# Kernel tuning notes

Hardware: AMD Instinct MI355X
Metric: run time of the kernel (lower is better)

Reference implementation:

```python
import jax, jax.numpy as jnp
from jax import lax
import numpy as np

STATE_DIM = 64
CHANNELS = 128
SEQ_LEN = 4096
BATCH = 16
DT_MIN, DT_MAX = 1e-3, 1e-1


def hippo(n):
    # HiPPO-LegS construction, matching the torch staticmethod
    ar = jnp.arange(n, dtype=jnp.float32)
    P = jnp.sqrt(1.0 + 2.0 * ar)
    A = P[:, None] * P[None, :]
    A = jnp.tril(A) - jnp.diag(ar)
    B = jnp.sqrt(2.0 * ar + 1.0)
    return -A, B[:, None]


def setup_inputs() -> dict:
    key = jax.random.key(0)
    k_u, k_c = jax.random.split(key)
    A, B = hippo(STATE_DIM)
    # xavier_normal_ for C: std = sqrt(2/(fan_in+fan_out))
    std = float(np.sqrt(2.0 / (CHANNELS + STATE_DIM)))
    C = jax.random.normal(k_c, (CHANNELS, STATE_DIM), dtype=jnp.float32) * std
    D = jnp.ones((CHANNELS, 1), dtype=jnp.float32)
    # deterministic dt at log-midpoint of [dt_min, dt_max]
    dt = jnp.exp(jnp.array([(np.log(DT_MIN) + np.log(DT_MAX)) / 2.0], dtype=jnp.float32))
    u = jax.random.normal(k_u, (BATCH, SEQ_LEN), dtype=jnp.float32)
    return {"u": u, "A": A, "B": B, "C": C, "D": D, "dt": dt}


def reference(u, A, B, C, D, dt):
    # Training-path forward of LinearStateSpaceLayer (conv-kernel construction + conv1d)
    b, L = u.shape
    n = A.shape[0]
    dt_s = dt[0]
    I = jnp.eye(n, dtype=A.dtype)
    BL = jnp.linalg.inv(I - 0.5 * dt_s * A)            # bilinear discretization
    A_bar = BL @ (I + 0.5 * dt_s * A)                  # (n, n)
    B_bar = (BL * dt_s) @ B                            # (n, 1)

    # kernel k[j] = C @ A_bar^j @ B_bar for j = 0..L-1, via a scan of matvecs
    def step(v, _):
        return A_bar @ v, v
    _, vs = lax.scan(step, B_bar[:, 0], None, length=L)  # (L, n), vs[j] = A_bar^j B_bar
    k_causal = vs @ C.T                                  # (L, channels)
    # torch ordering: k_conv[c, 0, i] = C A_bar^{L-1-i} B_bar = k_causal[L-1-i, c]
    k_conv = k_causal[::-1].T[:, None, :]                # (channels, 1, L)

    # torch F.conv1d is cross-correlation; lax conv_general_dilated matches
    y = lax.conv_general_dilated(
        u[:, None, :], k_conv,
        window_strides=(1,), padding=[(L - 1, L - 1)],
        dimension_numbers=("NCH", "OIH", "NCH"),
    )[:, :, :L]                                          # (b, channels, L)

    # skip term: (u.unsqueeze(-1) @ D.T).transpose(-1,-2) == u[b,t] * D[c,0]
    y = y + u[:, None, :] * D[None, :, :]                # (b, channels, L)
    return y
```

## Files before the change

kernel.cpp:

```cpp
#include <hip/hip_runtime.h>

#define NS   64
#define CH   128
#define LSEQ 4096
#define NB   16
#define SCH  64
#define MCH  64
#define ST   68
#define CP   128

#define WS_ABAR 0
#define WS_A16  4096
#define WS_VS   8192
#define WS_BBAR 12288

#define X0_IDX(b, m) (((size_t)(b) * CH) * LSEQ + (size_t)(m) * SCH)

#define P_VSS  0
#define P_XCW  1024
#define P_XBS  1280
#define P_PLE  1536
#define P_PART 1792
#define P_A16  2048

#define FMA44(av, bv)                                                          \
    a0.x += av.x * bv.x; a0.y += av.x * bv.y; a0.z += av.x * bv.z; a0.w += av.x * bv.w; \
    a1.x += av.y * bv.x; a1.y += av.y * bv.y; a1.z += av.y * bv.z; a1.w += av.y * bv.w; \
    a2.x += av.z * bv.x; a2.y += av.z * bv.y; a2.z += av.z * bv.z; a2.w += av.z * bv.w; \
    a3.x += av.w * bv.x; a3.y += av.w * bv.y; a3.z += av.w * bv.z; a3.w += av.w * bv.w;

__global__ __launch_bounds__(512) void k_sb(const float* __restrict__ u,
                                            const float* __restrict__ A,
                                            const float* __restrict__ Bv,
                                            const float* __restrict__ dtp,
                                            float* __restrict__ ws,
                                            float* __restrict__ out) {
    __shared__ __align__(16) float Mrow[NS * ST];
    __shared__ __align__(16) float Mcol[(NS + 1) * ST];
    __shared__ __align__(16) float Nrow[NS * ST];
    __shared__ __align__(16) float Ncol[NS * ST];
    __shared__ __align__(16) float VT[NS * ST];
    __shared__ __align__(16) float vsS[NS * NS];
    __shared__ __align__(16) float xleS[MCH * NS];
    __shared__ __align__(16) float part[2][4 * NS];
    __shared__ __align__(16) float bcol[NS];
    __shared__ float rdiag[NS], xcS[NS];
    const int tid = threadIdx.x;
    const int b = blockIdx.x;
    const float dt = dtp[0];
    const float hdt = 0.5f * dt;

    for (int o = tid; o < NS * ST; o += 512) { Mrow[o] = 0.f; Nrow[o] = 0.f; Ncol[o] = 0.f; VT[o] = 0.f; }
    for (int o = tid; o < (NS + 1) * ST; o += 512) Mcol[o] = 0.f;
    __syncthreads();

    for (int o = tid; o < NS * NS; o += 512) {
        int i = o >> 6, k = o & 63;
        float a = A[o];
        float d = (i == k) ? 1.0f : 0.0f;
        Nrow[i * ST + k] = d - hdt * a;
        Ncol[k * ST + i] = d + hdt * a;
    }
    if (tid < NS) {
        bcol[tid]  = dt * Bv[tid];
        rdiag[tid] = 1.0f / (1.0f - hdt * A[tid * NS + tid]);
    }
    __syncthreads();

    if (tid <= NS) {
        float xr[NS];
        const float* t2b = (tid < NS) ? &Ncol[tid * ST] : bcol;
#pragma unroll
        for (int I = 0; I < 16; ++I) {
            const int i0 = 4 * I;
            float4 t2 = *(const float4*)&t2b[i0];
            float a0 = t2.x, a1 = t2.y, a2 = t2.z, a3 = t2.w;
#pragma unroll
            for (int k = 0; k < i0; k += 4) {
                float4 n0 = *(const float4*)&Nrow[(i0 + 0) * ST + k];
                float4 n1 = *(const float4*)&Nrow[(i0 + 1) * ST + k];
                float4 n2 = *(const float4*)&Nrow[(i0 + 2) * ST + k];
                float4 n3 = *(const float4*)&Nrow[(i0 + 3) * ST + k];
                a0 -= n0.x * xr[k] + n0.y * xr[k + 1] + n0.z * xr[k + 2] + n0.w * xr[k + 3];
                a1 -= n1.x * xr[k] + n1.y * xr[k + 1] + n1.z * xr[k + 2] + n1.w * xr[k + 3];
                a2 -= n2.x * xr[k] + n2.y * xr[k + 1] + n2.z * xr[k + 2] + n2.w * xr[k + 3];
                a3 -= n3.x * xr[k] + n3.y * xr[k + 1] + n3.z * xr[k + 2] + n3.w * xr[k + 3];
            }
            float4 rd  = *(const float4*)&rdiag[i0];
            float4 nb1 = *(const float4*)&Nrow[(i0 + 1) * ST + i0];
            float4 nb2 = *(const float4*)&Nrow[(i0 + 2) * ST + i0];
            float4 nb3 = *(const float4*)&Nrow[(i0 + 3) * ST + i0];
            float x0 = a0 * rd.x;
            float x1 = (a1 - nb1.x * x0) * rd.y;
            float x2 = (a2 - nb2.x * x0 - nb2.y * x1) * rd.z;
            float x3 = (a3 - nb3.x * x0 - nb3.y * x1 - nb3.z * x2) * rd.w;
            xr[i0 + 0] = x0; xr[i0 + 1] = x1; xr[i0 + 2] = x2; xr[i0 + 3] = x3;
        }
        float* xrow = &Mcol[tid * ST];
#pragma unroll
        for (int k = 0; k < NS; k += 4) {
            float4 v = {xr[k], xr[k + 1], xr[k + 2], xr[k + 3]};
            *(float4*)&xrow[k] = v;
        }
    }
    __syncthreads();

    if (tid < 256) {
        const int i0 = 4 * (tid >> 4), j0 = 4 * (tid & 15);
        float4 r0 = *(const float4*)&Mcol[(j0 + 0) * ST + i0];
        float4 r1 = *(const float4*)&Mcol[(j0 + 1) * ST + i0];
        float4 r2 = *(const float4*)&Mcol[(j0 + 2) * ST + i0];
        float4 r3 = *(const float4*)&Mcol[(j0 + 3) * ST + i0];
        float4 w0 = {r0.x, r1.x, r2.x, r3.x};
        float4 w1 = {r0.y, r1.y, r2.y, r3.y};
        float4 w2 = {r0.z, r1.z, r2.z, r3.z};
        float4 w3 = {r0.w, r1.w, r2.w, r3.w};
        *(float4*)&Mrow[(i0 + 0) * ST + j0] = w0;
        *(float4*)&Mrow[(i0 + 1) * ST + j0] = w1;
        *(float4*)&Mrow[(i0 + 2) * ST + j0] = w2;
        *(float4*)&Mrow[(i0 + 3) * ST + j0] = w3;
        if (b == 0) {
            *(float4*)&ws[WS_ABAR + (i0 + 0) * NS + j0] = w0;
            *(float4*)&ws[WS_ABAR + (i0 + 1) * NS + j0] = w1;
            *(float4*)&ws[WS_ABAR + (i0 + 2) * NS + j0] = w2;
            *(float4*)&ws[WS_ABAR + (i0 + 3) * NS + j0] = w3;
        }
    }
    if (b == 0 && tid < 16)
        *(float4*)&ws[WS_BBAR + 4 * tid] = *(const float4*)&Mcol[NS * ST + 4 * tid];
    if (tid < NS) VT[tid * ST + 0] = Mcol[NS * ST + tid];
    __syncthreads();

    float *cm = Mrow, *cmt = Mcol, *nm = Nrow, *nmt = Ncol;
    const int l = tid & 63;
    const int si0 = 16 * ((tid >> 6) & 3) + 4 * (l >> 4);
    const int sj0 = 4 * (l & 15);
    for (int s = 1; s <= 6; ++s) {
        if (tid < 256) {
            float4 a0 = {0,0,0,0}, a1 = {0,0,0,0}, a2 = {0,0,0,0}, a3 = {0,0,0,0};
#pragma unroll 4
            for (int k = 0; k < NS; k += 4) {
                float4 av0 = *(const float4*)&cmt[(k + 0) * ST + si0];
                float4 bv0 = *(const float4*)&cm [(k + 0) * ST + sj0];
                float4 av1 = *(const float4*)&cmt[(k + 1) * ST + si0];
                float4 bv1 = *(const float4*)&cm [(k + 1) * ST + sj0];
                float4 av2 = *(const float4*)&cmt[(k + 2) * ST + si0];
                float4 bv2 = *(const float4*)&cm [(k + 2) * ST + sj0];
                float4 av3 = *(const float4*)&cmt[(k + 3) * ST + si0];
                float4 bv3 = *(const float4*)&cm [(k + 3) * ST + sj0];
                FMA44(av0, bv0)
                FMA44(av1, bv1)
                FMA44(av2, bv2)
                FMA44(av3, bv3)
            }
            *(float4*)&nm[(si0 + 0) * ST + sj0] = a0;
            *(float4*)&nm[(si0 + 1) * ST + sj0] = a1;
            *(float4*)&nm[(si0 + 2) * ST + sj0] = a2;
            *(float4*)&nm[(si0 + 3) * ST + sj0] = a3;
            float4 t0 = {a0.x, a1.x, a2.x, a3.x};
            float4 t1 = {a0.y, a1.y, a2.y, a3.y};
            float4 t2 = {a0.z, a1.z, a2.z, a3.z};
            float4 t3 = {a0.w, a1.w, a2.w, a3.w};
            *(float4*)&nmt[(sj0 + 0) * ST + si0] = t0;
            *(float4*)&nmt[(sj0 + 1) * ST + si0] = t1;
            *(float4*)&nmt[(sj0 + 2) * ST + si0] = t2;
            *(float4*)&nmt[(sj0 + 3) * ST + si0] = t3;
        } else {
            const int e = tid - 256;
            if (s == 1) {
                if (e < NS) {
                    float sum = 0.f;
#pragma unroll 8
                    for (int k = 0; k < NS; ++k) sum += cmt[k * ST + e] * VT[k * ST + 0];
                    VT[e * ST + 1] = sum;
                }
            } else if (s == 2) {
                if (e < 2 * NS) {
                    const int i = e & 63, j = e >> 6;
                    float sum = 0.f;
#pragma unroll 8
                    for (int k = 0; k < NS; ++k) sum += cmt[k * ST + i] * VT[k * ST + j];
                    VT[i * ST + 2 + j] = sum;
                }
            } else {
                const int mexp = 1 << (s - 1);
                if (e < 4 * mexp) {
                    const int vi = 4 * (e & 15), vj = 4 * (e >> 4);
                    float4 a0 = {0,0,0,0}, a1 = {0,0,0,0}, a2 = {0,0,0,0}, a3 = {0,0,0,0};
#pragma unroll 4
                    for (int k = 0; k < NS; k += 2) {
                        float4 av  = *(const float4*)&cmt[k * ST + vi];
                        float4 bv  = *(const float4*)&VT [k * ST + vj];
                        float4 av2 = *(const float4*)&cmt[(k + 1) * ST + vi];
                        float4 bv2 = *(const float4*)&VT [(k + 1) * ST + vj];
                        FMA44(av, bv)
                        FMA44(av2, bv2)
                    }
                    *(float4*)&VT[(vi + 0) * ST + vj + mexp] = a0;
                    *(float4*)&VT[(vi + 1) * ST + vj + mexp] = a1;
                    *(float4*)&VT[(vi + 2) * ST + vj + mexp] = a2;
                    *(float4*)&VT[(vi + 3) * ST + vj + mexp] = a3;
                }
            }
        }
        __syncthreads();
        { float* t = cm; cm = nm; nm = t; t = cmt; cmt = nmt; nmt = t; }
        if (s == 4 && b == 0) {
            for (int o = tid; o < (NS * NS) / 4; o += 512) {
                int r = o >> 4, c4 = (o & 15) * 4;
                *(float4*)&ws[WS_A16 + r * NS + c4] = *(const float4*)&cm[r * ST + c4];
            }
        }
    }

    if (tid < 256) {
        const int i0 = 4 * (tid >> 4), j0 = 4 * (tid & 15);
        float4 v0 = *(const float4*)&VT[(i0 + 0) * ST + j0];
        float4 v1 = *(const float4*)&VT[(i0 + 1) * ST + j0];
        float4 v2 = *(const float4*)&VT[(i0 + 2) * ST + j0];
        float4 v3 = *(const float4*)&VT[(i0 + 3) * ST + j0];
        float4 w0 = {v0.x, v1.x, v2.x, v3.x};
        float4 w1 = {v0.y, v1.y, v2.y, v3.y};
        float4 w2 = {v0.z, v1.z, v2.z, v3.z};
        float4 w3 = {v0.w, v1.w, v2.w, v3.w};
        *(float4*)&vsS[(j0 + 0) * NS + i0] = w0;
        *(float4*)&vsS[(j0 + 1) * NS + i0] = w1;
        *(float4*)&vsS[(j0 + 2) * NS + i0] = w2;
        *(float4*)&vsS[(j0 + 3) * NS + i0] = w3;
        if (b == 0) {
            *(float4*)&ws[WS_VS + (j0 + 0) * NS + i0] = w0;
            *(float4*)&ws[WS_VS + (j0 + 1) * NS + i0] = w1;
            *(float4*)&ws[WS_VS + (j0 + 2) * NS + i0] = w2;
            *(float4*)&ws[WS_VS + (j0 + 3) * NS + i0] = w3;
        }
    }
    {
        const int jj = tid & 63;
#pragma unroll
        for (int rep = 0; rep < 2; ++rep) {
            const int m0 = 4 * (tid >> 6) + 32 * rep;
            float4 v;
            v.x = u[b * LSEQ + (m0 + 0) * SCH + 63 - jj];
            v.y = u[b * LSEQ + (m0 + 1) * SCH + 63 - jj];
            v.z = u[b * LSEQ + (m0 + 2) * SCH + 63 - jj];
            v.w = u[b * LSEQ + (m0 + 3) * SCH + 63 - jj];
            *(float4*)&Nrow[jj * ST + m0] = v;
        }
    }
    const int i = tid & 63, q = (tid >> 6) & 3;
    float4 a64[4];
    if (tid < 256) {
#pragma unroll
        for (int kq = 0; kq < 4; ++kq)
            a64[kq] = *(const float4*)&Mrow[i * ST + 16 * q + 4 * kq];
    }
    if (tid < NS) xcS[tid] = 0.f;
    __syncthreads();

    if (tid < 256) {
        const int ig = tid & 15, mg = tid >> 4;
        float4 a0 = {0,0,0,0}, a1 = {0,0,0,0}, a2 = {0,0,0,0}, a3 = {0,0,0,0};
#pragma unroll 4
        for (int j = 0; j < NS; j += 2) {
            float4 am  = *(const float4*)&Nrow[j * ST + 4 * mg];
            float4 bi  = *(const float4*)&vsS[j * NS + 4 * ig];
            float4 am2 = *(const float4*)&Nrow[(j + 1) * ST + 4 * mg];
            float4 bi2 = *(const float4*)&vsS[(j + 1) * NS + 4 * ig];
            FMA44(am, bi)
            FMA44(am2, bi2)
        }
        *(float4*)&xleS[(4 * mg + 0) * NS + 4 * ig] = a0;
        *(float4*)&xleS[(4 * mg + 1) * NS + 4 * ig] = a1;
        *(float4*)&xleS[(4 * mg + 2) * NS + 4 * ig] = a2;
        *(float4*)&xleS[(4 * mg + 3) * NS + 4 * ig] = a3;
    }
    __syncthreads();

    for (int m = 0; m < MCH; ++m) {
        if (tid < 256) {
            if (q == 0 && tid < 64) out[X0_IDX(b, m) + i] = xcS[i];
            float4 t0 = *(const float4*)(xcS + 16 * q + 0);
            float4 t1 = *(const float4*)(xcS + 16 * q + 4);
            float4 t2 = *(const float4*)(xcS + 16 * q + 8);
            float4 t3 = *(const float4*)(xcS + 16 * q + 12);
            float s = a64[0].x * t0.x + a64[0].y * t0.y + a64[0].z * t0.z + a64[0].w * t0.w
                    + a64[1].x * t1.x + a64[1].y * t1.y + a64[1].z * t1.z + a64[1].w * t1.w
                    + a64[2].x * t2.x + a64[2].y * t2.y + a64[2].z * t2.z + a64[2].w * t2.w
                    + a64[3].x * t3.x + a64[3].y * t3.y + a64[3].z * t3.z + a64[3].w * t3.w;
            part[m & 1][q * 64 + i] = s;
        }
        __syncthreads();
        if (tid < 256) {
            float xn = part[m & 1][i] + part[m & 1][64 + i] + part[m & 1][128 + i]
                     + part[m & 1][192 + i] + xleS[m * 64 + i];
            xcS[i] = xn;
        }
    }
}

__global__ __launch_bounds__(256) void k_main2(const float* __restrict__ u,
                                               const float* __restrict__ Cm,
                                               const float* __restrict__ Dv,
                                               const float* __restrict__ ws,
                                               float* __restrict__ out) {
    __shared__ __align__(16) float Xl[NS * ST];
    __shared__ __align__(16) float pool[NS * CP];
    __shared__ float uS[SCH], DS[CH], bbS[NS];
    const int m = blockIdx.x, b = blockIdx.y;
    const int tid = threadIdx.x;
    const int l = tid & 63, w = tid >> 6;

    for (int o = tid; o < (NS * NS) / 4; o += 256) {
        int r = o >> 4, c4 = (o & 15) * 4;
        *(float4*)&Xl[r * ST + c4]          = *(const float4*)&ws[WS_ABAR + r * NS + c4];
        *(float4*)&pool[P_A16 + r * NS + c4] = *(const float4*)&ws[WS_A16 + r * NS + c4];
    }
    for (int o = tid; o < 16 * NS; o += 256) pool[P_VSS + o] = ws[WS_VS + o];
    if (tid < NS) {
        uS[tid]  = u[b * LSEQ + m * SCH + tid];
        bbS[tid] = ws[WS_BBAR + tid];
        pool[P_XBS + tid] = out[X0_IDX(b, m) + tid];
    }
    if (tid < CH) DS[tid] = Dv[tid];
    __syncthreads();

    const int r0 = l & 15, q = l >> 4;
    float4 ar[4][4];
#pragma unroll
    for (int b4 = 0; b4 < 4; ++b4)
#pragma unroll
        for (int kq = 0; kq < 4; ++kq)
            ar[b4][kq] = *(const float4*)&Xl[(r0 + 16 * b4) * ST + 16 * q + 4 * kq];
    float bbr[4];
#pragma unroll
    for (int b4 = 0; b4 < 4; ++b4) bbr[b4] = bbS[r0 + 16 * b4];
    float4 a16r[4];
#pragma unroll
    for (int kq = 0; kq < 4; ++kq)
        a16r[kq] = *(const float4*)&pool[P_A16 + l * NS + 16 * w + 4 * kq];

    {
        float s = 0.f;
#pragma unroll
        for (int j = 0; j < 16; ++j) s += pool[P_VSS + j * NS + l] * uS[16 * w + 15 - j];
        pool[P_PLE + w * NS + l] = s;
    }
    __syncthreads();

    for (int p = 1; p < 4; ++p) {
        float4 x0q = *(const float4*)&pool[P_XBS + (p - 1) * NS + 16 * w + 0];
        float4 x1q = *(const float4*)&pool[P_XBS + (p - 1) * NS + 16 * w + 4];
        float4 x2q = *(const float4*)&pool[P_XBS + (p - 1) * NS + 16 * w + 8];
        float4 x3q = *(const float4*)&pool[P_XBS + (p - 1) * NS + 16 * w + 12];
        float s = a16r[0].x * x0q.x + a16r[0].y * x0q.y + a16r[0].z * x0q.z + a16r[0].w * x0q.w
                + a16r[1].x * x1q.x + a16r[1].y * x1q.y + a16r[1].z * x1q.z + a16r[1].w * x1q.w
                + a16r[2].x * x2q.x + a16r[2].y * x2q.y + a16r[2].z * x2q.z + a16r[2].w * x2q.w
                + a16r[3].x * x3q.x + a16r[3].y * x3q.y + a16r[3].z * x3q.z + a16r[3].w * x3q.w;
        pool[P_PART + w * NS + l] = s;
        __syncthreads();
        if (w == 0) {
            float xn = pool[P_PART + l] + pool[P_PART + NS + l] + pool[P_PART + 2 * NS + l]
                     + pool[P_PART + 3 * NS + l] + pool[P_PLE + (p - 1) * NS + l];
            pool[P_XBS + p * NS + l] = xn;
        }
        __syncthreads();
    }

    pool[P_XCW + w * NS + l] = pool[P_XBS + w * NS + l];
    for (int s = 0; s < 16; ++s) {
        __threadfence_block();
        const int t = 16 * w + s;
        float4 x0q = *(const float4*)&pool[P_XCW + w * NS + 16 * q + 0];
        float4 x1q = *(const float4*)&pool[P_XCW + w * NS + 16 * q + 4];
        float4 x2q = *(const float4*)&pool[P_XCW + w * NS + 16 * q + 8];
        float4 x3q = *(const float4*)&pool[P_XCW + w * NS + 16 * q + 12];
        float p0, p1, p2, p3;
        p0 = ar[0][0].x * x0q.x + ar[0][0].y * x0q.y + ar[0][0].z * x0q.z + ar[0][0].w * x0q.w
           + ar[0][1].x * x1q.x + ar[0][1].y * x1q.y + ar[0][1].z * x1q.z + ar[0][1].w * x1q.w
           + ar[0][2].x * x2q.x + ar[0][2].y * x2q.y + ar[0][2].z * x2q.z + ar[0][2].w * x2q.w
           + ar[0][3].x * x3q.x + ar[0][3].y * x3q.y + ar[0][3].z * x3q.z + ar[0][3].w * x3q.w;
        p1 = ar[1][0].x * x0q.x + ar[1][0].y * x0q.y + ar[1][0].z * x0q.z + ar[1][0].w * x0q.w
           + ar[1][1].x * x1q.x + ar[1][1].y * x1q.y + ar[1][1].z * x1q.z + ar[1][1].w * x1q.w
           + ar[1][2].x * x2q.x + ar[1][2].y * x2q.y + ar[1][2].z * x2q.z + ar[1][2].w * x2q.w
           + ar[1][3].x * x3q.x + ar[1][3].y * x3q.y + ar[1][3].z * x3q.z + ar[1][3].w * x3q.w;
        p2 = ar[2][0].x * x0q.x + ar[2][0].y * x0q.y + ar[2][0].z * x0q.z + ar[2][0].w * x0q.w
           + ar[2][1].x * x1q.x + ar[2][1].y * x1q.y + ar[2][1].z * x1q.z + ar[2][1].w * x1q.w
           + ar[2][2].x * x2q.x + ar[2][2].y * x2q.y + ar[2][2].z * x2q.z + ar[2][2].w * x2q.w
           + ar[2][3].x * x3q.x + ar[2][3].y * x3q.y + ar[2][3].z * x3q.z + ar[2][3].w * x3q.w;
        p3 = ar[3][0].x * x0q.x + ar[3][0].y * x0q.y + ar[3][0].z * x0q.z + ar[3][0].w * x0q.w
           + ar[3][1].x * x1q.x + ar[3][1].y * x1q.y + ar[3][1].z * x1q.z + ar[3][1].w * x1q.w
           + ar[3][2].x * x2q.x + ar[3][2].y * x2q.y + ar[3][2].z * x2q.z + ar[3][2].w * x2q.w
           + ar[3][3].x * x3q.x + ar[3][3].y * x3q.y + ar[3][3].z * x3q.z + ar[3][3].w * x3q.w;
        p0 += __shfl_xor(p0, 16, 64); p1 += __shfl_xor(p1, 16, 64);
        p2 += __shfl_xor(p2, 16, 64); p3 += __shfl_xor(p3, 16, 64);
        p0 += __shfl_xor(p0, 32, 64); p1 += __shfl_xor(p1, 32, 64);
        p2 += __shfl_xor(p2, 32, 64); p3 += __shfl_xor(p3, 32, 64);
        const float ut = uS[t];
        p0 += bbr[0] * ut; p1 += bbr[1] * ut; p2 += bbr[2] * ut; p3 += bbr[3] * ut;
        const float xv = (q == 0) ? p0 : (q == 1) ? p1 : (q == 2) ? p2 : p3;
        const int row = r0 + 16 * q;
        pool[P_XCW + w * NS + row] = xv;
        Xl[row * ST + t] = xv;
    }
    __syncthreads();

#pragma unroll
    for (int rep = 0; rep < 8; ++rep) {
        const int ii = tid & 63;
        const int cg = (tid >> 6) + 4 * rep;
        float4 v;
        v.x = Cm[(4 * cg + 0) * NS + ii];
        v.y = Cm[(4 * cg + 1) * NS + ii];
        v.z = Cm[(4 * cg + 2) * NS + ii];
        v.w = Cm[(4 * cg + 3) * NS + ii];
        *(float4*)&pool[ii * CP + 4 * cg] = v;
    }
    __syncthreads();

    {
        const int tg = tid & 7, cq = tid >> 3;
        float acc[4][8];
#pragma unroll
        for (int r = 0; r < 4; ++r)
#pragma unroll
            for (int c = 0; c < 8; ++c) acc[r][c] = 0.f;
#pragma unroll 4
        for (int ii = 0; ii < NS; ++ii) {
            float4 cv = *(const float4*)&pool[ii * CP + 4 * cq];
            float4 xa = *(const float4*)&Xl[ii * ST + 8 * tg + 0];
            float4 xb = *(const float4*)&Xl[ii * ST + 8 * tg + 4];
            float cr[4] = {cv.x, cv.y, cv.z, cv.w};
            float xv[8] = {xa.x, xa.y, xa.z, xa.w, xb.x, xb.y, xb.z, xb.w};
#pragma unroll
            for (int r = 0; r < 4; ++r)
#pragma unroll
                for (int c = 0; c < 8; ++c) acc[r][c] += cr[r] * xv[c];
        }
        const size_t obase = ((size_t)b * CH) * LSEQ + (size_t)m * SCH + 8 * tg;
#pragma unroll
        for (int r = 0; r < 4; ++r) {
            const int c = 4 * cq + r;
            const float dv = DS[c];
            float4 o1, o2;
            o1.x = acc[r][0] + dv * uS[8 * tg + 0];
            o1.y = acc[r][1] + dv * uS[8 * tg + 1];
            o1.z = acc[r][2] + dv * uS[8 * tg + 2];
            o1.w = acc[r][3] + dv * uS[8 * tg + 3];
            o2.x = acc[r][4] + dv * uS[8 * tg + 4];
            o2.y = acc[r][5] + dv * uS[8 * tg + 5];
            o2.z = acc[r][6] + dv * uS[8 * tg + 6];
            o2.w = acc[r][7] + dv * uS[8 * tg + 7];
            float* op = out + obase + (size_t)c * LSEQ;
            *(float4*)(op)     = o1;
            *(float4*)(op + 4) = o2;
        }
    }
}

extern "C" void kernel_launch(void* const* d_in, const int* in_sizes, int n_in,
                              void* d_out, int out_size, void* d_ws, size_t ws_size,
                              hipStream_t stream) {
    const float* u   = (const float*)d_in[0];
    const float* A   = (const float*)d_in[1];
    const float* Bv  = (const float*)d_in[2];
    const float* Cm  = (const float*)d_in[3];
    const float* Dv  = (const float*)d_in[4];
    const float* dtp = (const float*)d_in[5];
    float* ws  = (float*)d_ws;
    float* out = (float*)d_out;

    k_sb<<<NB, 512, 0, stream>>>(u, A, Bv, dtp, ws, out);
    k_main2<<<dim3(MCH, NB), 256, 0, stream>>>(u, Cm, Dv, ws, out);
}
```

Before: 161.0 us.

## Replace serial chunk-state recurrence with log-depth parallel prefix scan

```diff
diff --git a/kernel.cpp b/kernel.cpp
--- a/kernel.cpp
+++ b/kernel.cpp
@@ -28,6 +28,82 @@
     a1.x += av.y * bv.x; a1.y += av.y * bv.y; a1.z += av.y * bv.z; a1.w += av.y * bv.w; \
     a2.x += av.z * bv.x; a2.y += av.z * bv.y; a2.z += av.z * bv.z; a2.w += av.z * bv.w; \
     a3.x += av.w * bv.x; a3.y += av.w * bv.y; a3.z += av.w * bv.z; a3.w += av.w * bv.w;
+
+__device__ __forceinline__ void mm_square(const float* __restrict__ cm,
+                                          const float* __restrict__ cmt,
+                                          float* __restrict__ nm,
+                                          float* __restrict__ nmt, int tid) {
+    const int l = tid & 63;
+    const int si0 = 16 * ((tid >> 6) & 3) + 4 * (l >> 4);
+    const int sj0 = 4 * (l & 15);
+    float4 a0 = {0,0,0,0}, a1 = {0,0,0,0}, a2 = {0,0,0,0}, a3 = {0,0,0,0};
+#pragma unroll 4
+    for (int k = 0; k < NS; k += 4) {
+        float4 av0 = *(const float4*)&cmt[(k + 0) * ST + si0];
+        float4 bv0 = *(const float4*)&cm [(k + 0) * ST + sj0];
+        float4 av1 = *(const float4*)&cmt[(k + 1) * ST + si0];
+        float4 bv1 = *(const float4*)&cm [(k + 1) * ST + sj0];
+        float4 av2 = *(const float4*)&cmt[(k + 2) * ST + si0];
+        float4 bv2 = *(const float4*)&cm [(k + 2) * ST + sj0];
+        float4 av3 = *(const float4*)&cmt[(k + 3) * ST + si0];
+        float4 bv3 = *(const float4*)&cm [(k + 3) * ST + sj0];
+        FMA44(av0, bv0)
+        FMA44(av1, bv1)
+        FMA44(av2, bv2)
+        FMA44(av3, bv3)
+    }
+    *(float4*)&nm[(si0 + 0) * ST + sj0] = a0;
+    *(float4*)&nm[(si0 + 1) * ST + sj0] = a1;
+    *(float4*)&nm[(si0 + 2) * ST + sj0] = a2;
+    *(float4*)&nm[(si0 + 3) * ST + sj0] = a3;
+    float4 t0 = {a0.x, a1.x, a2.x, a3.x};
+    float4 t1 = {a0.y, a1.y, a2.y, a3.y};
+    float4 t2 = {a0.z, a1.z, a2.z, a3.z};
+    float4 t3 = {a0.w, a1.w, a2.w, a3.w};
+    *(float4*)&nmt[(sj0 + 0) * ST + si0] = t0;
+    *(float4*)&nmt[(sj0 + 1) * ST + si0] = t1;
+    *(float4*)&nmt[(sj0 + 2) * ST + si0] = t2;
+    *(float4*)&nmt[(sj0 + 3) * ST + si0] = t3;
+}
+
+template<int D>
+__device__ __forceinline__ void scan_level(const float* __restrict__ PT,
+                                           const float* __restrict__ Tin,
+                                           float* __restrict__ Tout, int e) {
+    const int i0 = 4 * (e >> 4);
+    const int m0 = 4 * (e & 15);
+    float4 a0 = {0,0,0,0}, a1 = {0,0,0,0}, a2 = {0,0,0,0}, a3 = {0,0,0,0};
+    if (D < 4 || m0 >= D) {
+#pragma unroll 4
+        for (int k = 0; k < NS; ++k) {
+            float4 av = *(const float4*)&PT[k * ST + i0];
+            float4 bv;
+            if constexpr (D >= 4) {
+                bv = *(const float4*)&Tin[k * ST + m0 - D];
+            } else {
+                float4 bhi = *(const float4*)&Tin[k * ST + m0];
+                float4 blo;
+                if (m0 >= 4) blo = *(const float4*)&Tin[k * ST + m0 - 4];
+                else { blo.x = 0.f; blo.y = 0.f; blo.z = 0.f; blo.w = 0.f; }
+                if constexpr (D == 1) { bv.x = blo.w; bv.y = bhi.x; bv.z = bhi.y; bv.w = bhi.z; }
+                else                  { bv.x = blo.z; bv.y = blo.w; bv.z = bhi.x; bv.w = bhi.y; }
+            }
+            FMA44(av, bv)
+        }
+    }
+    float4 t0 = *(const float4*)&Tin[(i0 + 0) * ST + m0];
+    float4 t1 = *(const float4*)&Tin[(i0 + 1) * ST + m0];
+    float4 t2 = *(const float4*)&Tin[(i0 + 2) * ST + m0];
+    float4 t3 = *(const float4*)&Tin[(i0 + 3) * ST + m0];
+    a0.x += t0.x; a0.y += t0.y; a0.z += t0.z; a0.w += t0.w;
+    a1.x += t1.x; a1.y += t1.y; a1.z += t1.z; a1.w += t1.w;
+    a2.x += t2.x; a2.y += t2.y; a2.z += t2.z; a2.w += t2.w;
+    a3.x += t3.x; a3.y += t3.y; a3.z += t3.z; a3.w += t3.w;
+    *(float4*)&Tout[(i0 + 0) * ST + m0] = a0;
+    *(float4*)&Tout[(i0 + 1) * ST + m0] = a1;
+    *(float4*)&Tout[(i0 + 2) * ST + m0] = a2;
+    *(float4*)&Tout[(i0 + 3) * ST + m0] = a3;
+}
 
 __global__ __launch_bounds__(512) void k_sb(const float* __restrict__ u,
                                             const float* __restrict__ A,
@@ -39,12 +115,13 @@
     __shared__ __align__(16) float Mcol[(NS + 1) * ST];
     __shared__ __align__(16) float Nrow[NS * ST];
     __shared__ __align__(16) float Ncol[NS * ST];
+    __shared__ __align__(16) float Wrow[NS * ST];
+    __shared__ __align__(16) float Wcol[NS * ST];
     __shared__ __align__(16) float VT[NS * ST];
-    __shared__ __align__(16) float vsS[NS * NS];
-    __shared__ __align__(16) float xleS[MCH * NS];
-    __shared__ __align__(16) float part[2][4 * NS];
+    __shared__ __align__(16) float T1[NS * ST];
     __shared__ __align__(16) float bcol[NS];
-    __shared__ float rdiag[NS], xcS[NS];
+    __shared__ float rdiag[NS];
+    float* const vsS = Wrow;
     const int tid = threadIdx.x;
     const int b = blockIdx.x;
     const float dt = dtp[0];
@@ -132,39 +209,9 @@
     __syncthreads();
 
     float *cm = Mrow, *cmt = Mcol, *nm = Nrow, *nmt = Ncol;
-    const int l = tid & 63;
-    const int si0 = 16 * ((tid >> 6) & 3) + 4 * (l >> 4);
-    const int sj0 = 4 * (l & 15);
     for (int s = 1; s <= 6; ++s) {
         if (tid < 256) {
-            float4 a0 = {0,0,0,0}, a1 = {0,0,0,0}, a2 = {0,0,0,0}, a3 = {0,0,0,0};
-#pragma unroll 4
-            for (int k = 0; k < NS; k += 4) {
-                float4 av0 = *(const float4*)&cmt[(k + 0) * ST + si0];
-                float4 bv0 = *(const float4*)&cm [(k + 0) * ST + sj0];
-                float4 av1 = *(const float4*)&cmt[(k + 1) * ST + si0];
-                float4 bv1 = *(const float4*)&cm [(k + 1) * ST + sj0];
-                float4 av2 = *(const float4*)&cmt[(k + 2) * ST + si0];
-                float4 bv2 = *(const float4*)&cm [(k + 2) * ST + sj0];
-                float4 av3 = *(const float4*)&cmt[(k + 3) * ST + si0];
-                float4 bv3 = *(const float4*)&cm [(k + 3) * ST + sj0];
-                FMA44(av0, bv0)
-                FMA44(av1, bv1)
-                FMA44(av2, bv2)
-                FMA44(av3, bv3)
-            }
-            *(float4*)&nm[(si0 + 0) * ST + sj0] = a0;
-            *(float4*)&nm[(si0 + 1) * ST + sj0] = a1;
-            *(float4*)&nm[(si0 + 2) * ST + sj0] = a2;
-            *(float4*)&nm[(si0 + 3) * ST + sj0] = a3;
-            float4 t0 = {a0.x, a1.x, a2.x, a3.x};
-            float4 t1 = {a0.y, a1.y, a2.y, a3.y};
-            float4 t2 = {a0.z, a1.z, a2.z, a3.z};
-            float4 t3 = {a0.w, a1.w, a2.w, a3.w};
-            *(float4*)&nmt[(sj0 + 0) * ST + si0] = t0;
-            *(float4*)&nmt[(sj0 + 1) * ST + si0] = t1;
-            *(float4*)&nmt[(sj0 + 2) * ST + si0] = t2;
-            *(float4*)&nmt[(sj0 + 3) * ST + si0] = t3;
+            mm_square(cm, cmt, nm, nmt, tid);
         } else {
             const int e = tid - 256;
             if (s == 1) {
@@ -244,57 +291,78 @@
             v.y = u[b * LSEQ + (m0 + 1) * SCH + 63 - jj];
             v.z = u[b * LSEQ + (m0 + 2) * SCH + 63 - jj];
             v.w = u[b * LSEQ + (m0 + 3) * SCH + 63 - jj];
-            *(float4*)&Nrow[jj * ST + m0] = v;
-        }
-    }
-    const int i = tid & 63, q = (tid >> 6) & 3;
-    float4 a64[4];
+            *(float4*)&T1[jj * ST + m0] = v;
+        }
+    }
+    __syncthreads();
+
     if (tid < 256) {
-#pragma unroll
-        for (int kq = 0; kq < 4; ++kq)
-            a64[kq] = *(const float4*)&Mrow[i * ST + 16 * q + 4 * kq];
-    }
-    if (tid < NS) xcS[tid] = 0.f;
-    __syncthreads();
-
-    if (tid < 256) {
-        const int ig = tid & 15, mg = tid >> 4;
+        mm_square(Mrow, Mcol, Nrow, Ncol, tid);
+    } else {
+        const int e = tid - 256;
+        const int ig = e & 15, mg = e >> 4;
         float4 a0 = {0,0,0,0}, a1 = {0,0,0,0}, a2 = {0,0,0,0}, a3 = {0,0,0,0};
 #pragma unroll 4
         for (int j = 0; j < NS; j += 2) {
-            float4 am  = *(const float4*)&Nrow[j * ST + 4 * mg];
+            float4 am  = *(const float4*)&T1[j * ST + 4 * mg];
             float4 bi  = *(const float4*)&vsS[j * NS + 4 * ig];
-            float4 am2 = *(const float4*)&Nrow[(j + 1) * ST + 4 * mg];
+            float4 am2 = *(const float4*)&T1[(j + 1) * ST + 4 * mg];
             float4 bi2 = *(const float4*)&vsS[(j + 1) * NS + 4 * ig];
             FMA44(am, bi)
             FMA44(am2, bi2)
         }
-        *(float4*)&xleS[(4 * mg + 0) * NS + 4 * ig] = a0;
-        *(float4*)&xleS[(4 * mg + 1) * NS + 4 * ig] = a1;
-        *(float4*)&xleS[(4 * mg + 2) * NS + 4 * ig] = a2;
-        *(float4*)&xleS[(4 * mg + 3) * NS + 4 * ig] = a3;
-    }
-    __syncthreads();
-
-    for (int m = 0; m < MCH; ++m) {
-        if (tid < 256) {
-            if (q == 0 && tid < 64) out[X0_IDX(b, m) + i] = xcS[i];
-            float4 t0 = *(const float4*)(xcS + 16 * q + 0);
-            float4 t1 = *(const float4*)(xcS + 16 * q + 4);
-            float4 t2 = *(const float4*)(xcS + 16 * q + 8);
-            float4 t3 = *(const float4*)(xcS + 16 * q + 12);
-            float s = a64[0].x * t0.x + a64[0].y * t0.y + a64[0].z * t0.z + a64[0].w * t0.w
-                    + a64[1].x * t1.x + a64[1].y * t1.y + a64[1].z * t1.z + a64[1].w * t1.w
-                    + a64[2].x * t2.x + a64[2].y * t2.y + a64[2].z * t2.z + a64[2].w * t2.w
-                    + a64[3].x * t3.x + a64[3].y * t3.y + a64[3].z * t3.z + a64[3].w * t3.w;
-            part[m & 1][q * 64 + i] = s;
-        }
-        __syncthreads();
-        if (tid < 256) {
-            float xn = part[m & 1][i] + part[m & 1][64 + i] + part[m & 1][128 + i]
-                     + part[m & 1][192 + i] + xleS[m * 64 + i];
-            xcS[i] = xn;
-        }
+        float4 w0 = {a0.x, a1.x, a2.x, a3.x};
+        float4 w1 = {a0.y, a1.y, a2.y, a3.y};
+        float4 w2 = {a0.z, a1.z, a2.z, a3.z};
+        float4 w3 = {a0.w, a1.w, a2.w, a3.w};
+        *(float4*)&VT[(4 * ig + 0) * ST + 4 * mg] = w0;
+        *(float4*)&VT[(4 * ig + 1) * ST + 4 * mg] = w1;
+        *(float4*)&VT[(4 * ig + 2) * ST + 4 * mg] = w2;
+        *(float4*)&VT[(4 * ig + 3) * ST + 4 * mg] = w3;
+    }
+    __syncthreads();
+
+    if (tid < 256) mm_square(Nrow, Ncol, Wrow, Wcol, tid);
+    else           scan_level<1>(Mcol, VT, T1, tid - 256);
+    __syncthreads();
+
+    if (tid < 256) mm_square(Wrow, Wcol, Mrow, Mcol, tid);
+    else           scan_level<2>(Ncol, T1, VT, tid - 256);
+    __syncthreads();
+
+    if (tid < 256) mm_square(Mrow, Mcol, Nrow, Ncol, tid);
+    else           scan_level<4>(Wcol, VT, T1, tid - 256);
+    __syncthreads();
+
+    if (tid < 256) mm_square(Nrow, Ncol, Wrow, Wcol, tid);
+    else           scan_level<8>(Mcol, T1, VT, tid - 256);
+    __syncthreads();
+
+    if (tid >= 256) scan_level<16>(Ncol, VT, T1, tid - 256);
+    __syncthreads();
+
+    if (tid >= 256) scan_level<32>(Wcol, T1, VT, tid - 256);
+    __syncthreads();
+
+    {
+        const int m = tid >> 3;
+        const int i0 = (tid & 7) * 8;
+        float4 o1, o2;
+        if (m == 0) {
+            o1.x = o1.y = o1.z = o1.w = 0.f;
+            o2.x = o2.y = o2.z = o2.w = 0.f;
+        } else {
+            o1.x = VT[(i0 + 0) * ST + m - 1];
+            o1.y = VT[(i0 + 1) * ST + m - 1];
+            o1.z = VT[(i0 + 2) * ST + m - 1];
+            o1.w = VT[(i0 + 3) * ST + m - 1];
+            o2.x = VT[(i0 + 4) * ST + m - 1];
+            o2.y = VT[(i0 + 5) * ST + m - 1];
+            o2.z = VT[(i0 + 6) * ST + m - 1];
+            o2.w = VT[(i0 + 7) * ST + m - 1];
+        }
+        *(float4*)&out[X0_IDX(b, m) + i0]     = o1;
+        *(float4*)&out[X0_IDX(b, m) + i0 + 4] = o2;
     }
 }
 
```

New measurement: 171.7 us. 1.07x slower.

## Run chunk-state recurrence in a single wavefront with shuffles instead of block syncs

Applied to the files above, without the earlier changes.

```diff
diff --git a/kernel.cpp b/kernel.cpp
--- a/kernel.cpp
+++ b/kernel.cpp
@@ -40,19 +40,15 @@
     __shared__ __align__(16) float Nrow[NS * ST];
     __shared__ __align__(16) float Ncol[NS * ST];
     __shared__ __align__(16) float VT[NS * ST];
+    __shared__ __align__(16) float uT[NS * ST];
     __shared__ __align__(16) float vsS[NS * NS];
     __shared__ __align__(16) float xleS[MCH * NS];
-    __shared__ __align__(16) float part[2][4 * NS];
     __shared__ __align__(16) float bcol[NS];
-    __shared__ float rdiag[NS], xcS[NS];
+    __shared__ float rdiag[NS];
     const int tid = threadIdx.x;
     const int b = blockIdx.x;
     const float dt = dtp[0];
     const float hdt = 0.5f * dt;
-
-    for (int o = tid; o < NS * ST; o += 512) { Mrow[o] = 0.f; Nrow[o] = 0.f; Ncol[o] = 0.f; VT[o] = 0.f; }
-    for (int o = tid; o < (NS + 1) * ST; o += 512) Mcol[o] = 0.f;
-    __syncthreads();
 
     for (int o = tid; o < NS * NS; o += 512) {
         int i = o >> 6, k = o & 63;
@@ -66,6 +62,20 @@
         rdiag[tid] = 1.0f / (1.0f - hdt * A[tid * NS + tid]);
     }
     __syncthreads();
+
+    {
+        const int jj = tid & 63;
+#pragma unroll
+        for (int rep = 0; rep < 2; ++rep) {
+            const int m0 = 4 * (tid >> 6) + 32 * rep;
+            float4 v;
+            v.x = u[b * LSEQ + (m0 + 0) * SCH + 63 - jj];
+            v.y = u[b * LSEQ + (m0 + 1) * SCH + 63 - jj];
+            v.z = u[b * LSEQ + (m0 + 2) * SCH + 63 - jj];
+            v.w = u[b * LSEQ + (m0 + 3) * SCH + 63 - jj];
+            *(float4*)&uT[jj * ST + m0] = v;
+        }
+    }
 
     if (tid <= NS) {
         float xr[NS];
@@ -234,27 +244,6 @@
             *(float4*)&ws[WS_VS + (j0 + 3) * NS + i0] = w3;
         }
     }
-    {
-        const int jj = tid & 63;
-#pragma unroll
-        for (int rep = 0; rep < 2; ++rep) {
-            const int m0 = 4 * (tid >> 6) + 32 * rep;
-            float4 v;
-            v.x = u[b * LSEQ + (m0 + 0) * SCH + 63 - jj];
-            v.y = u[b * LSEQ + (m0 + 1) * SCH + 63 - jj];
-            v.z = u[b * LSEQ + (m0 + 2) * SCH + 63 - jj];
-            v.w = u[b * LSEQ + (m0 + 3) * SCH + 63 - jj];
-            *(float4*)&Nrow[jj * ST + m0] = v;
-        }
-    }
-    const int i = tid & 63, q = (tid >> 6) & 3;
-    float4 a64[4];
-    if (tid < 256) {
-#pragma unroll
-        for (int kq = 0; kq < 4; ++kq)
-            a64[kq] = *(const float4*)&Mrow[i * ST + 16 * q + 4 * kq];
-    }
-    if (tid < NS) xcS[tid] = 0.f;
     __syncthreads();
 
     if (tid < 256) {
@@ -262,9 +251,9 @@
         float4 a0 = {0,0,0,0}, a1 = {0,0,0,0}, a2 = {0,0,0,0}, a3 = {0,0,0,0};
 #pragma unroll 4
         for (int j = 0; j < NS; j += 2) {
-            float4 am  = *(const float4*)&Nrow[j * ST + 4 * mg];
+            float4 am  = *(const float4*)&uT[j * ST + 4 * mg];
             float4 bi  = *(const float4*)&vsS[j * NS + 4 * ig];
-            float4 am2 = *(const float4*)&Nrow[(j + 1) * ST + 4 * mg];
+            float4 am2 = *(const float4*)&uT[(j + 1) * ST + 4 * mg];
             float4 bi2 = *(const float4*)&vsS[(j + 1) * NS + 4 * ig];
             FMA44(am, bi)
             FMA44(am2, bi2)
@@ -276,24 +265,28 @@
     }
     __syncthreads();
 
-    for (int m = 0; m < MCH; ++m) {
-        if (tid < 256) {
-            if (q == 0 && tid < 64) out[X0_IDX(b, m) + i] = xcS[i];
-            float4 t0 = *(const float4*)(xcS + 16 * q + 0);
-            float4 t1 = *(const float4*)(xcS + 16 * q + 4);
-            float4 t2 = *(const float4*)(xcS + 16 * q + 8);
-            float4 t3 = *(const float4*)(xcS + 16 * q + 12);
-            float s = a64[0].x * t0.x + a64[0].y * t0.y + a64[0].z * t0.z + a64[0].w * t0.w
-                    + a64[1].x * t1.x + a64[1].y * t1.y + a64[1].z * t1.z + a64[1].w * t1.w
-                    + a64[2].x * t2.x + a64[2].y * t2.y + a64[2].z * t2.z + a64[2].w * t2.w
-                    + a64[3].x * t3.x + a64[3].y * t3.y + a64[3].z * t3.z + a64[3].w * t3.w;
-            part[m & 1][q * 64 + i] = s;
-        }
-        __syncthreads();
-        if (tid < 256) {
-            float xn = part[m & 1][i] + part[m & 1][64 + i] + part[m & 1][128 + i]
-                     + part[m & 1][192 + i] + xleS[m * 64 + i];
-            xcS[i] = xn;
+    if (tid < 64) {
+        const int i = tid;
+        float arow[NS];
+#pragma unroll
+        for (int c = 0; c < NS; c += 4) {
+            float4 v = *(const float4*)&Mrow[i * ST + c];
+            arow[c + 0] = v.x; arow[c + 1] = v.y; arow[c + 2] = v.z; arow[c + 3] = v.w;
+        }
+        float* xp = out + ((size_t)b * CH) * LSEQ + i;
+        float x = 0.f;
+        for (int m = 0; m < MCH; ++m) {
+            xp[(size_t)m * SCH] = x;
+            const float xv = xleS[m * NS + i];
+            float a0 = 0.f, a1 = 0.f, a2 = 0.f, a3 = 0.f;
+#pragma unroll
+            for (int j = 0; j < NS; j += 4) {
+                a0 = fmaf(arow[j + 0], __shfl(x, j + 0, 64), a0);
+                a1 = fmaf(arow[j + 1], __shfl(x, j + 1, 64), a1);
+                a2 = fmaf(arow[j + 2], __shfl(x, j + 2, 64), a2);
+                a3 = fmaf(arow[j + 3], __shfl(x, j + 3, 64), a3);
+            }
+            x = ((a0 + a1) + (a2 + a3)) + xv;
         }
     }
 }
```

Result: slower. 166.4 us (+3.4%).

## Replace 64-step serial chunk recurrence with blocked stride-4 scan using A_bar^256

Applied to the files above, without the earlier changes.

```diff
diff --git a/kernel.cpp b/kernel.cpp
--- a/kernel.cpp
+++ b/kernel.cpp
@@ -28,6 +28,81 @@
     a1.x += av.y * bv.x; a1.y += av.y * bv.y; a1.z += av.y * bv.z; a1.w += av.y * bv.w; \
     a2.x += av.z * bv.x; a2.y += av.z * bv.y; a2.z += av.z * bv.z; a2.w += av.z * bv.w; \
     a3.x += av.w * bv.x; a3.y += av.w * bv.y; a3.z += av.w * bv.z; a3.w += av.w * bv.w;
+
+template<bool WT>
+__device__ __forceinline__ void mm_square(const float* __restrict__ cm,
+                                          const float* __restrict__ cmt,
+                                          float* __restrict__ nm,
+                                          float* __restrict__ nmt, int e) {
+    const int l = e & 63;
+    const int si0 = 16 * ((e >> 6) & 3) + 4 * (l >> 4);
+    const int sj0 = 4 * (l & 15);
+    float4 a0 = {0,0,0,0}, a1 = {0,0,0,0}, a2 = {0,0,0,0}, a3 = {0,0,0,0};
+#pragma unroll 4
+    for (int k = 0; k < NS; k += 4) {
+        float4 av0 = *(const float4*)&cmt[(k + 0) * ST + si0];
+        float4 bv0 = *(const float4*)&cm [(k + 0) * ST + sj0];
+        float4 av1 = *(const float4*)&cmt[(k + 1) * ST + si0];
+        float4 bv1 = *(const float4*)&cm [(k + 1) * ST + sj0];
+        float4 av2 = *(const float4*)&cmt[(k + 2) * ST + si0];
+        float4 bv2 = *(const float4*)&cm [(k + 2) * ST + sj0];
+        float4 av3 = *(const float4*)&cmt[(k + 3) * ST + si0];
+        float4 bv3 = *(const float4*)&cm [(k + 3) * ST + sj0];
+        FMA44(av0, bv0)
+        FMA44(av1, bv1)
+        FMA44(av2, bv2)
+        FMA44(av3, bv3)
+    }
+    *(float4*)&nm[(si0 + 0) * ST + sj0] = a0;
+    *(float4*)&nm[(si0 + 1) * ST + sj0] = a1;
+    *(float4*)&nm[(si0 + 2) * ST + sj0] = a2;
+    *(float4*)&nm[(si0 + 3) * ST + sj0] = a3;
+    if (WT) {
+        float4 t0 = {a0.x, a1.x, a2.x, a3.x};
+        float4 t1 = {a0.y, a1.y, a2.y, a3.y};
+        float4 t2 = {a0.z, a1.z, a2.z, a3.z};
+        float4 t3 = {a0.w, a1.w, a2.w, a3.w};
+        *(float4*)&nmt[(sj0 + 0) * ST + si0] = t0;
+        *(float4*)&nmt[(sj0 + 1) * ST + si0] = t1;
+        *(float4*)&nmt[(sj0 + 2) * ST + si0] = t2;
+        *(float4*)&nmt[(sj0 + 3) * ST + si0] = t3;
+    }
+}
+
+template<int R>
+__device__ __forceinline__ void horner_step(const float* __restrict__ Acol,
+                                            const float* __restrict__ xle,
+                                            const float* __restrict__ Hprev,
+                                            float* __restrict__ Hcur, int e) {
+    const int g = e >> 4, i0 = 4 * (e & 15);
+    const float* bp = (R == 1) ? &xle[(4 * g) * NS] : &Hprev[g * ST];
+    float4 acc = *(const float4*)&xle[(4 * g + R) * NS + i0];
+#pragma unroll 8
+    for (int k = 0; k < NS; ++k) {
+        float4 av = *(const float4*)&Acol[k * ST + i0];
+        float bk = bp[k];
+        acc.x = fmaf(av.x, bk, acc.x); acc.y = fmaf(av.y, bk, acc.y);
+        acc.z = fmaf(av.z, bk, acc.z); acc.w = fmaf(av.w, bk, acc.w);
+    }
+    *(float4*)&Hcur[g * ST + i0] = acc;
+}
+
+__device__ __forceinline__ void inner_step(const float* __restrict__ Acol,
+                                           const float* __restrict__ xle,
+                                           float* __restrict__ stash, int r, int e) {
+    const int g = e >> 4, i0 = 4 * (e & 15);
+    const int mp = 4 * g + r - 1;
+    float4 acc = *(const float4*)&xle[mp * NS + i0];
+    const float* xp = &stash[mp * ST];
+#pragma unroll 8
+    for (int k = 0; k < NS; ++k) {
+        float4 av = *(const float4*)&Acol[k * ST + i0];
+        float xk = xp[k];
+        acc.x = fmaf(av.x, xk, acc.x); acc.y = fmaf(av.y, xk, acc.y);
+        acc.z = fmaf(av.z, xk, acc.z); acc.w = fmaf(av.w, xk, acc.w);
+    }
+    *(float4*)&stash[(mp + 1) * ST + i0] = acc;
+}
 
 __global__ __launch_bounds__(512) void k_sb(const float* __restrict__ u,
                                             const float* __restrict__ A,
@@ -40,19 +115,19 @@
     __shared__ __align__(16) float Nrow[NS * ST];
     __shared__ __align__(16) float Ncol[NS * ST];
     __shared__ __align__(16) float VT[NS * ST];
+    __shared__ __align__(16) float uT[NS * ST];
     __shared__ __align__(16) float vsS[NS * NS];
     __shared__ __align__(16) float xleS[MCH * NS];
     __shared__ __align__(16) float part[2][4 * NS];
     __shared__ __align__(16) float bcol[NS];
     __shared__ float rdiag[NS], xcS[NS];
+    float* const stash = uT;
+    float* const Hb0 = vsS;
+    float* const Hb1 = vsS + 16 * ST;
     const int tid = threadIdx.x;
     const int b = blockIdx.x;
     const float dt = dtp[0];
     const float hdt = 0.5f * dt;
-
-    for (int o = tid; o < NS * ST; o += 512) { Mrow[o] = 0.f; Nrow[o] = 0.f; Ncol[o] = 0.f; VT[o] = 0.f; }
-    for (int o = tid; o < (NS + 1) * ST; o += 512) Mcol[o] = 0.f;
-    __syncthreads();
 
     for (int o = tid; o < NS * NS; o += 512) {
         int i = o >> 6, k = o & 63;
@@ -66,6 +141,20 @@
         rdiag[tid] = 1.0f / (1.0f - hdt * A[tid * NS + tid]);
     }
     __syncthreads();
+
+    {
+        const int jj = tid & 63;
+#pragma unroll
+        for (int rep = 0; rep < 2; ++rep) {
+            const int m0 = 4 * (tid >> 6) + 32 * rep;
+            float4 v;
+            v.x = u[b * LSEQ + (m0 + 0) * SCH + 63 - jj];
+            v.y = u[b * LSEQ + (m0 + 1) * SCH + 63 - jj];
+            v.z = u[b * LSEQ + (m0 + 2) * SCH + 63 - jj];
+            v.w = u[b * LSEQ + (m0 + 3) * SCH + 63 - jj];
+            *(float4*)&uT[jj * ST + m0] = v;
+        }
+    }
 
     if (tid <= NS) {
         float xr[NS];
@@ -132,39 +221,9 @@
     __syncthreads();
 
     float *cm = Mrow, *cmt = Mcol, *nm = Nrow, *nmt = Ncol;
-    const int l = tid & 63;
-    const int si0 = 16 * ((tid >> 6) & 3) + 4 * (l >> 4);
-    const int sj0 = 4 * (l & 15);
     for (int s = 1; s <= 6; ++s) {
         if (tid < 256) {
-            float4 a0 = {0,0,0,0}, a1 = {0,0,0,0}, a2 = {0,0,0,0}, a3 = {0,0,0,0};
-#pragma unroll 4
-            for (int k = 0; k < NS; k += 4) {
-                float4 av0 = *(const float4*)&cmt[(k + 0) * ST + si0];
-                float4 bv0 = *(const float4*)&cm [(k + 0) * ST + sj0];
-                float4 av1 = *(const float4*)&cmt[(k + 1) * ST + si0];
-                float4 bv1 = *(const float4*)&cm [(k + 1) * ST + sj0];
-                float4 av2 = *(const float4*)&cmt[(k + 2) * ST + si0];
-                float4 bv2 = *(const float4*)&cm [(k + 2) * ST + sj0];
-                float4 av3 = *(const float4*)&cmt[(k + 3) * ST + si0];
-                float4 bv3 = *(const float4*)&cm [(k + 3) * ST + sj0];
-                FMA44(av0, bv0)
-                FMA44(av1, bv1)
-                FMA44(av2, bv2)
-                FMA44(av3, bv3)
-            }
-            *(float4*)&nm[(si0 + 0) * ST + sj0] = a0;
-            *(float4*)&nm[(si0 + 1) * ST + sj0] = a1;
-            *(float4*)&nm[(si0 + 2) * ST + sj0] = a2;
-            *(float4*)&nm[(si0 + 3) * ST + sj0] = a3;
-            float4 t0 = {a0.x, a1.x, a2.x, a3.x};
-            float4 t1 = {a0.y, a1.y, a2.y, a3.y};
-            float4 t2 = {a0.z, a1.z, a2.z, a3.z};
-            float4 t3 = {a0.w, a1.w, a2.w, a3.w};
-            *(float4*)&nmt[(sj0 + 0) * ST + si0] = t0;
-            *(float4*)&nmt[(sj0 + 1) * ST + si0] = t1;
-            *(float4*)&nmt[(sj0 + 2) * ST + si0] = t2;
-            *(float4*)&nmt[(sj0 + 3) * ST + si0] = t3;
+            mm_square<true>(cm, cmt, nm, nmt, tid);
         } else {
             const int e = tid - 256;
             if (s == 1) {
@@ -233,28 +292,9 @@
             *(float4*)&ws[WS_VS + (j0 + 2) * NS + i0] = w2;
             *(float4*)&ws[WS_VS + (j0 + 3) * NS + i0] = w3;
         }
-    }
-    {
-        const int jj = tid & 63;
-#pragma unroll
-        for (int rep = 0; rep < 2; ++rep) {
-            const int m0 = 4 * (tid >> 6) + 32 * rep;
-            float4 v;
-            v.x = u[b * LSEQ + (m0 + 0) * SCH + 63 - jj];
-            v.y = u[b * LSEQ + (m0 + 1) * SCH + 63 - jj];
-            v.z = u[b * LSEQ + (m0 + 2) * SCH + 63 - jj];
-            v.w = u[b * LSEQ + (m0 + 3) * SCH + 63 - jj];
-            *(float4*)&Nrow[jj * ST + m0] = v;
-        }
-    }
-    const int i = tid & 63, q = (tid >> 6) & 3;
-    float4 a64[4];
-    if (tid < 256) {
-#pragma unroll
-        for (int kq = 0; kq < 4; ++kq)
-            a64[kq] = *(const float4*)&Mrow[i * ST + 16 * q + 4 * kq];
-    }
-    if (tid < NS) xcS[tid] = 0.f;
+    } else {
+        mm_square<true>(Mrow, Mcol, Nrow, Ncol, tid - 256);
+    }
     __syncthreads();
 
     if (tid < 256) {
@@ -262,9 +302,9 @@
         float4 a0 = {0,0,0,0}, a1 = {0,0,0,0}, a2 = {0,0,0,0}, a3 = {0,0,0,0};
 #pragma unroll 4
         for (int j = 0; j < NS; j += 2) {
-            float4 am  = *(const float4*)&Nrow[j * ST + 4 * mg];
+            float4 am  = *(const float4*)&uT[j * ST + 4 * mg];
             float4 bi  = *(const float4*)&vsS[j * NS + 4 * ig];
-            float4 am2 = *(const float4*)&Nrow[(j + 1) * ST + 4 * mg];
+            float4 am2 = *(const float4*)&uT[(j + 1) * ST + 4 * mg];
             float4 bi2 = *(const float4*)&vsS[(j + 1) * NS + 4 * ig];
             FMA44(am, bi)
             FMA44(am2, bi2)
@@ -273,28 +313,64 @@
         *(float4*)&xleS[(4 * mg + 1) * NS + 4 * ig] = a1;
         *(float4*)&xleS[(4 * mg + 2) * NS + 4 * ig] = a2;
         *(float4*)&xleS[(4 * mg + 3) * NS + 4 * ig] = a3;
-    }
-    __syncthreads();
-
-    for (int m = 0; m < MCH; ++m) {
-        if (tid < 256) {
-            if (q == 0 && tid < 64) out[X0_IDX(b, m) + i] = xcS[i];
-            float4 t0 = *(const float4*)(xcS + 16 * q + 0);
-            float4 t1 = *(const float4*)(xcS + 16 * q + 4);
-            float4 t2 = *(const float4*)(xcS + 16 * q + 8);
-            float4 t3 = *(const float4*)(xcS + 16 * q + 12);
-            float s = a64[0].x * t0.x + a64[0].y * t0.y + a64[0].z * t0.z + a64[0].w * t0.w
-                    + a64[1].x * t1.x + a64[1].y * t1.y + a64[1].z * t1.z + a64[1].w * t1.w
-                    + a64[2].x * t2.x + a64[2].y * t2.y + a64[2].z * t2.z + a64[2].w * t2.w
-                    + a64[3].x * t3.x + a64[3].y * t3.y + a64[3].z * t3.z + a64[3].w * t3.w;
-            part[m & 1][q * 64 + i] = s;
-        }
+    } else {
+        mm_square<false>(Nrow, Ncol, VT, VT, tid - 256);
+    }
+    __syncthreads();
+
+    float4 a256[4];
+    if (tid < 256) {
+        const int i = tid & 63, q = tid >> 6;
+#pragma unroll
+        for (int kq = 0; kq < 4; ++kq)
+            a256[kq] = *(const float4*)&VT[i * ST + 16 * q + 4 * kq];
+        horner_step<1>(Mcol, xleS, Hb0, Hb0, tid);
+    } else if (tid < 320) {
+        xcS[tid - 256] = 0.f;
+        stash[tid - 256] = 0.f;
+    }
+    __syncthreads();
+    if (tid < 256) horner_step<2>(Mcol, xleS, Hb0, Hb1, tid);
+    __syncthreads();
+    if (tid < 256) horner_step<3>(Mcol, xleS, Hb1, Hb0, tid);
+    __syncthreads();
+
+    {
+        const int i = tid & 63, q = (tid >> 6) & 3;
+        for (int g = 0; g < 15; ++g) {
+            if (tid < 256) {
+                float4 t0 = *(const float4*)(xcS + 16 * q + 0);
+                float4 t1 = *(const float4*)(xcS + 16 * q + 4);
+                float4 t2 = *(const float4*)(xcS + 16 * q + 8);
+                float4 t3 = *(const float4*)(xcS + 16 * q + 12);
+                float s = a256[0].x * t0.x + a256[0].y * t0.y + a256[0].z * t0.z + a256[0].w * t0.w
+                        + a256[1].x * t1.x + a256[1].y * t1.y + a256[1].z * t1.z + a256[1].w * t1.w
+                        + a256[2].x * t2.x + a256[2].y * t2.y + a256[2].z * t2.z + a256[2].w * t2.w
+                        + a256[3].x * t3.x + a256[3].y * t3.y + a256[3].z * t3.z + a256[3].w * t3.w;
+                part[g & 1][q * 64 + i] = s;
+            }
+            __syncthreads();
+            if (tid < 256) {
+                float xn = part[g & 1][i] + part[g & 1][64 + i] + part[g & 1][128 + i]
+                         + part[g & 1][192 + i] + Hb0[g * ST + i];
+                xcS[i] = xn;
+                stash[(4 * g + 4) * ST + i] = xn;
+            }
+        }
+    }
+    __syncthreads();
+
+    for (int r = 1; r <= 3; ++r) {
+        if (tid < 256) inner_step(Mcol, xleS, stash, r, tid);
         __syncthreads();
-        if (tid < 256) {
-            float xn = part[m & 1][i] + part[m & 1][64 + i] + part[m & 1][128 + i]
-                     + part[m & 1][192 + i] + xleS[m * 64 + i];
-            xcS[i] = xn;
-        }
+    }
+
+    {
+        const int m = tid >> 3, t8 = (tid & 7) * 8;
+        float4 o1 = *(const float4*)&stash[m * ST + t8];
+        float4 o2 = *(const float4*)&stash[m * ST + t8 + 4];
+        *(float4*)&out[X0_IDX(b, m) + t8]     = o1;
+        *(float4*)&out[X0_IDX(b, m) + t8 + 4] = o2;
     }
 }
 
```

New measurement: 156.6 us. -2.7%, faster.
